# Kernel optimization log

Hardware: AMD Instinct MI355X
Metric: run time of the kernel (lower is better)

Reference implementation:

```python
import jax, jax.numpy as jnp
import numpy as np

N_NODES = 50000
N_EDGES = 300000
N_GRAPHS = 256
F_IN = 78
H1 = 10
F_H1 = 78
F_OUT = 128
NEG_SLOPE = 0.2  # PyG GATConv default leaky_relu slope


def gat_conv(x, src, dst, W, a_src, a_dst, bias, heads, out_dim):
    """PyG GATConv (eval mode): linear -> per-edge attention -> segment softmax over
    destination nodes -> scatter-add aggregation -> concat heads + bias.
    src/dst already include self-loops."""
    N = x.shape[0]
    h = (x @ W).reshape(N, heads, out_dim)              # [N,H,F]
    al_s = (h * a_src[None]).sum(-1)                     # [N,H]
    al_d = (h * a_dst[None]).sum(-1)                     # [N,H]
    e = jax.nn.leaky_relu(al_s[src] + al_d[dst], NEG_SLOPE)  # [E,H]
    m = jax.ops.segment_max(e, dst, num_segments=N)      # stable softmax per dst node
    w = jnp.exp(e - m[dst])
    denom = jax.ops.segment_sum(w, dst, num_segments=N)
    alpha = w / denom[dst]                               # [E,H]
    out = jax.ops.segment_sum(h[src] * alpha[:, :, None], dst, num_segments=N)
    return out.reshape(N, heads * out_dim) + bias


def setup_inputs() -> dict:
    key = jax.random.key(0)
    ks = jax.random.split(key, 16)
    x = jax.random.normal(ks[0], (N_NODES, F_IN), dtype=jnp.float32)
    edge_index = jax.random.randint(ks[1], (2, N_EDGES), 0, N_NODES, dtype=jnp.int32)
    batch = jnp.sort(jax.random.randint(ks[2], (N_NODES,), 0, N_GRAPHS, dtype=jnp.int32))
    s = 0.1
    W1 = jax.random.normal(ks[3], (F_IN, H1 * F_H1), dtype=jnp.float32) * s
    a_src1 = jax.random.normal(ks[4], (H1, F_H1), dtype=jnp.float32) * s
    a_dst1 = jax.random.normal(ks[5], (H1, F_H1), dtype=jnp.float32) * s
    b1 = jnp.zeros((H1 * F_H1,), dtype=jnp.float32)
    W2 = jax.random.normal(ks[6], (H1 * F_H1, F_OUT), dtype=jnp.float32) * s
    a_src2 = jax.random.normal(ks[7], (1, F_OUT), dtype=jnp.float32) * s
    a_dst2 = jax.random.normal(ks[8], (1, F_OUT), dtype=jnp.float32) * s
    b2 = jnp.zeros((F_OUT,), dtype=jnp.float32)
    fc_w = jax.random.normal(ks[9], (F_OUT, F_OUT), dtype=jnp.float32) * s
    fc_b = jnp.zeros((F_OUT,), dtype=jnp.float32)
    return dict(x=x, edge_index=edge_index, batch=batch, W1=W1, a_src1=a_src1,
                a_dst1=a_dst1, b1=b1, W2=W2, a_src2=a_src2, a_dst2=a_dst2, b2=b2,
                fc_w=fc_w, fc_b=fc_b)


def reference(x, edge_index, batch, W1, a_src1, a_dst1, b1, W2, a_src2, a_dst2, b2, fc_w, fc_b):
    N = x.shape[0]
    loop = jnp.arange(N, dtype=edge_index.dtype)
    src = jnp.concatenate([edge_index[0], loop])  # add self-loops (PyG default)
    dst = jnp.concatenate([edge_index[1], loop])
    # dropout layers are identity in eval mode
    h = jax.nn.elu(gat_conv(x, src, dst, W1, a_src1, a_dst1, b1, H1, F_H1))
    h = gat_conv(h, src, dst, W2, a_src2, a_dst2, b2, 1, F_OUT)
    h = jax.nn.relu(h)
    g = jax.ops.segment_max(h, batch, num_segments=N_GRAPHS)  # global max pool [B,F]
    out = jax.nn.relu(g @ fc_w + fc_b)
    return out
```

## Files before the change

kernel.cpp:

```cpp
#include <hip/hip_runtime.h>
#include <hip/hip_bf16.h>

#define N_NODES 50000
#define N_EDGES 300000
#define E_TOT   350000
#define N_GRAPHS 256
#define F_IN 78
#define H1 10
#define D1 780
#define F_OUT 128
#define KP 800
#define K1P 96
#define NEG_SLOPE 0.2f
#define NB 196

typedef float v4f __attribute__((ext_vector_type(4)));
typedef short v8s __attribute__((ext_vector_type(8)));

__device__ __forceinline__ int src_of(int e, const int* __restrict__ ei) {
  return (e < N_EDGES) ? ei[e] : (e - N_EDGES);
}
__device__ __forceinline__ int dst_of(int e, const int* __restrict__ ei) {
  return (e < N_EDGES) ? ei[N_EDGES + e] : (e - N_EDGES);
}


__global__ void k_deg(const int* __restrict__ ei, int* __restrict__ deg) {
  int e = blockIdx.x * 256 + threadIdx.x;
  if (e >= E_TOT) return;
  atomicAdd(&deg[dst_of(e, ei)], 1);
}

__global__ void k_scan1(const int* __restrict__ deg, int* __restrict__ part) {
  __shared__ int s[256];
  int t = threadIdx.x;
  int i = blockIdx.x * 256 + t;
  s[t] = (i < N_NODES) ? deg[i] : 0;
  __syncthreads();
  for (int d = 128; d > 0; d >>= 1) {
    if (t < d) s[t] += s[t + d];
    __syncthreads();
  }
  if (t == 0) part[blockIdx.x] = s[0];
}

__global__ void k_scan2(const int* __restrict__ part, int* __restrict__ ppref) {
  if (threadIdx.x == 0) {
    int run = 0;
    for (int i = 0; i < NB; ++i) { ppref[i] = run; run += part[i]; }
  }
}

__global__ void k_scan3(const int* __restrict__ deg, const int* __restrict__ ppref,
                        int* __restrict__ offs, int* __restrict__ cursor) {
  __shared__ int s[256];
  int t = threadIdx.x;
  int i = blockIdx.x * 256 + t;
  int v = (i < N_NODES) ? deg[i] : 0;
  s[t] = v;
  __syncthreads();
  for (int d = 1; d < 256; d <<= 1) {
    int u = (t >= d) ? s[t - d] : 0;
    __syncthreads();
    s[t] += u;
    __syncthreads();
  }
  int excl = s[t] - v;
  if (i < N_NODES) {
    int off = ppref[blockIdx.x] + excl;
    offs[i] = off;
    cursor[i] = off;
  }
}

__global__ void k_scatter(const int* __restrict__ ei, int* __restrict__ cursor,
                          int* __restrict__ src_s, int* __restrict__ dst_s) {
  int e = blockIdx.x * 256 + threadIdx.x;
  if (e >= E_TOT) return;
  int s = src_of(e, ei);
  int d = dst_of(e, ei);
  int pos = atomicAdd(&cursor[d], 1);
  src_s[pos] = s;
  dst_s[pos] = d;
}


__global__ void k_prep(const float* __restrict__ W1, const float* __restrict__ as1,
                       const float* __restrict__ ad1, float* __restrict__ was,
                       float* __restrict__ wad) {
  int i = blockIdx.x * 256 + threadIdx.x;
  if (i >= F_IN * H1) return;
  int k = i / H1, h = i - k * H1;
  const float* wrow = W1 + (size_t)k * D1 + h * 78;
  const float* ar = as1 + h * 78;
  const float* br = ad1 + h * 78;
  float s = 0.f, d = 0.f;
  for (int f = 0; f < 78; ++f) {
    float w = wrow[f];
    s = fmaf(w, ar[f], s);
    d = fmaf(w, br[f], d);
  }
  was[i] = s;
  wad[i] = d;
}


__global__ __launch_bounds__(320) void k_logits1(const float* __restrict__ x,
                                                 const float* __restrict__ was,
                                                 const float* __restrict__ wad,
                                                 float* __restrict__ als,
                                                 float* __restrict__ ald) {
  __shared__ float xs[32][81];
  __shared__ float wl[D1], wl2[D1];
  int tid = threadIdx.x;
  int n0 = blockIdx.x * 32;
  for (int i = tid; i < 32 * F_IN; i += 320) {
    int r = i / F_IN, k = i - r * F_IN;
    int n = n0 + r;
    xs[r][k] = (n < N_NODES) ? x[(size_t)n * F_IN + k] : 0.f;
  }
  for (int i = tid; i < D1; i += 320) { wl[i] = was[i]; wl2[i] = wad[i]; }
  __syncthreads();
  int r = tid / 10, h = tid - r * 10;
  int n = n0 + r;
  float s = 0.f, d = 0.f;
  for (int k = 0; k < F_IN; ++k) {
    float xv = xs[r][k];
    s = fmaf(xv, wl[k * 10 + h], s);
    d = fmaf(xv, wl2[k * 10 + h], d);
  }
  if (n < N_NODES) { als[n * 10 + h] = s; ald[n * 10 + h] = d; }
}


__global__ void k_w1e(const float* __restrict__ als1, const float* __restrict__ ald1,
                      const int* __restrict__ src_s, const int* __restrict__ dst_s,
                      float* __restrict__ w1) {
  int i = blockIdx.x * 256 + threadIdx.x;
  if (i >= E_TOT * H1) return;
  int pos = i / H1, h = i - pos * H1;
  float v = als1[src_s[pos] * H1 + h] + ald1[dst_s[pos] * H1 + h];
  v = (v > 0.f) ? v : NEG_SLOPE * v;
  w1[i] = __expf(v);
}


__global__ void k_w1t(const float* __restrict__ W1, __hip_bfloat16* __restrict__ T) {
  int i = blockIdx.x * 256 + threadIdx.x;
  if (i >= 800 * K1P) return;
  int r = i / K1P, k = i - r * K1P;
  float v = (r < D1 && k < F_IN) ? W1[(size_t)k * D1 + r] : 0.f;
  T[i] = __float2bfloat16(v);
}


__global__ void k_w2t(const float* __restrict__ W2, __hip_bfloat16* __restrict__ Bt) {
  int i = blockIdx.x * 256 + threadIdx.x;
  if (i >= F_OUT * KP) return;
  int c = i / KP, k = i - c * KP;
  float v = (k < D1) ? W2[(size_t)k * F_OUT + c] : 0.f;
  Bt[i] = __float2bfloat16(v);
}


__global__ __launch_bounds__(512, 4) void k_l12(const float* __restrict__ x,
                                                const float* __restrict__ w1,
                                                const int* __restrict__ src_s,
                                                const int* __restrict__ offs,
                                                const int* __restrict__ deg,
                                                const __hip_bfloat16* __restrict__ W1T,
                                                const float* __restrict__ b1,
                                                const __hip_bfloat16* __restrict__ W2T,
                                                const float* __restrict__ a_src2,
                                                const float* __restrict__ a_dst2,
                                                float* __restrict__ h2,
                                                float* __restrict__ als2,
                                                float* __restrict__ ald2) {
  __shared__ __align__(16) unsigned char lds[33792];
  __hip_bfloat16* xbb = (__hip_bfloat16*)lds;
  __hip_bfloat16* out1t = (__hip_bfloat16*)lds;
  float* h2t = (float*)(lds + 25600);
#define XB(h, g, k) xbb[((h) * 16 + (g)) * 104 + (k)]

  int tid = threadIdx.x, wid = tid >> 6, lane = tid & 63;
  int n0 = blockIdx.x * 16;
  int col16 = lane & 15, kq = (lane >> 4) * 8;

  {
    unsigned int* p = (unsigned int*)lds;
    for (int i = tid; i < H1 * 16 * 52; i += 512) p[i] = 0u;
  }
  __syncthreads();

  #pragma unroll
  for (int rep = 0; rep < 2; ++rep) {
    int g = wid * 2 + rep;
    int n = n0 + g;
    int o = __builtin_amdgcn_readfirstlane(offs[n]);
    int d = __builtin_amdgcn_readfirstlane(deg[n]);
    float acc[H1], acc2[H1];
    #pragma unroll
    for (int h = 0; h < H1; ++h) { acc[h] = 0.f; acc2[h] = 0.f; }

    float onesel = (lane == 14) ? 1.0f : 0.f;
    int j = 0;
    for (; j + 4 <= d; j += 4) {
      int e0 = o + j;
      int s0 = src_s[e0], s1 = src_s[e0 + 1], s2 = src_s[e0 + 2], s3 = src_s[e0 + 3];
      const float* x0 = x + (size_t)s0 * F_IN;
      const float* x1 = x + (size_t)s1 * F_IN;
      const float* x2 = x + (size_t)s2 * F_IN;
      const float* x3 = x + (size_t)s3 * F_IN;
      float xa0 = x0[lane], xa1 = x1[lane], xa2 = x2[lane], xa3 = x3[lane];
      float xb0 = (lane < 14) ? x0[64 + lane] : onesel;
      float xb1 = (lane < 14) ? x1[64 + lane] : onesel;
      float xb2 = (lane < 14) ? x2[64 + lane] : onesel;
      float xb3 = (lane < 14) ? x3[64 + lane] : onesel;
      const float* wp = w1 + (size_t)e0 * H1;
      #pragma unroll
      for (int h = 0; h < H1; ++h) {
        float wa = wp[h], wb = wp[10 + h], wc = wp[20 + h], wd = wp[30 + h];
        acc[h] = fmaf(wa, xa0, acc[h]);
        acc[h] = fmaf(wb, xa1, acc[h]);
        acc[h] = fmaf(wc, xa2, acc[h]);
        acc[h] = fmaf(wd, xa3, acc[h]);
        acc2[h] = fmaf(wa, xb0, acc2[h]);
        acc2[h] = fmaf(wb, xb1, acc2[h]);
        acc2[h] = fmaf(wc, xb2, acc2[h]);
        acc2[h] = fmaf(wd, xb3, acc2[h]);
      }
    }
    for (; j < d; ++j) {
      int e0 = o + j;
      int s0 = src_s[e0];
      const float* x0 = x + (size_t)s0 * F_IN;
      float xa0 = x0[lane];
      float xb0 = (lane < 14) ? x0[64 + lane] : onesel;
      const float* wp = w1 + (size_t)e0 * H1;
      #pragma unroll
      for (int h = 0; h < H1; ++h) {
        float wa = wp[h];
        acc[h] = fmaf(wa, xa0, acc[h]);
        acc2[h] = fmaf(wa, xb0, acc2[h]);
      }
    }
    #pragma unroll
    for (int h = 0; h < H1; ++h) {
      float inv = 1.f / __shfl(acc2[h], 14);
      XB(h, g, lane) = __float2bfloat16(acc[h] * inv);
      if (lane < 14) XB(h, g, 64 + lane) = __float2bfloat16(acc2[h] * inv);
    }
  }
  __syncthreads();

  const unsigned short* Bp1 = (const unsigned short*)W1T;
  v4f res[7];
  int nu = 0;
  for (int u = wid; u < 50; u += 8) {
    int h = u / 5, nt = u - (u / 5) * 5;
    v4f acc = (v4f){0.f, 0.f, 0.f, 0.f};
    #pragma unroll
    for (int kt = 0; kt < 3; ++kt) {
      v8s a = *reinterpret_cast<const v8s*>(&XB(h, col16, kt * 32 + kq));
      v8s b = *reinterpret_cast<const v8s*>(
          &Bp1[(size_t)(h * 78 + nt * 16 + col16) * K1P + kt * 32 + kq]);
      acc = __builtin_amdgcn_mfma_f32_16x16x32_bf16(a, b, acc, 0, 0, 0);
    }
    res[nu++] = acc;
  }
  __syncthreads();

  if (tid < 160) {
    int node = tid / 10, cc = (tid - node * 10) * 2;
    *(unsigned int*)&out1t[node * 800 + 780 + cc] = 0u;
  }
  nu = 0;
  for (int u = wid; u < 50; u += 8) {
    int h = u / 5, nt = u - (u / 5) * 5;
    v4f acc = res[nu++];
    int cl = nt * 16 + col16;
    if (cl < 78) {
      int c = h * 78 + cl;
      float bv = b1[c];
      #pragma unroll
      for (int r = 0; r < 4; ++r) {
        int node = (lane >> 4) * 4 + r;
        float v = acc[r] + bv;
        v = (v > 0.f) ? v : expm1f(v);
        out1t[node * 800 + c] = __float2bfloat16(v);
      }
    }
  }
  __syncthreads();

  const unsigned short* Bp2 = (const unsigned short*)W2T;
  v4f acc3 = (v4f){0.f, 0.f, 0.f, 0.f};
  #pragma unroll 5
  for (int kt = 0; kt < 25; ++kt) {
    int k = kt * 32 + kq;
    v8s a = *reinterpret_cast<const v8s*>(&out1t[col16 * 800 + k]);
    v8s b = *reinterpret_cast<const v8s*>(&Bp2[(size_t)(wid * 16 + col16) * KP + k]);
    acc3 = __builtin_amdgcn_mfma_f32_16x16x32_bf16(a, b, acc3, 0, 0, 0);
  }
  {
    int col = wid * 16 + col16;
    #pragma unroll
    for (int r = 0; r < 4; ++r) {
      int node = (lane >> 4) * 4 + r;
      h2[(size_t)(n0 + node) * F_OUT + col] = acc3[r];
      h2t[node * F_OUT + col] = acc3[r];
    }
  }
  __syncthreads();

  #pragma unroll
  for (int rep = 0; rep < 2; ++rep) {
    int nn = wid * 2 + rep;
    float v0 = h2t[nn * F_OUT + lane], v1 = h2t[nn * F_OUT + 64 + lane];
    float s = v0 * a_src2[lane] + v1 * a_src2[64 + lane];
    float dd = v0 * a_dst2[lane] + v1 * a_dst2[64 + lane];
    #pragma unroll
    for (int off = 32; off > 0; off >>= 1) {
      s += __shfl_down(s, off);
      dd += __shfl_down(dd, off);
    }
    if (lane == 0) { als2[n0 + nn] = s; ald2[n0 + nn] = dd; }
  }
#undef XB
}


__global__ void k_w2e(const float* __restrict__ als2, const float* __restrict__ ald2,
                      const int* __restrict__ src_s, const int* __restrict__ dst_s,
                      float* __restrict__ w2) {
  int pos = blockIdx.x * 256 + threadIdx.x;
  if (pos >= E_TOT) return;
  float v = als2[src_s[pos]] + ald2[dst_s[pos]];
  v = (v > 0.f) ? v : NEG_SLOPE * v;
  w2[pos] = __expf(v);
}


__global__ __launch_bounds__(512) void k_agg2f(const float* __restrict__ h2,
                                               const float* __restrict__ w2,
                                               const int* __restrict__ src_s,
                                               const int* __restrict__ offs,
                                               const int* __restrict__ deg,
                                               const float* __restrict__ b2,
                                               const int* __restrict__ batch,
                                               unsigned int* __restrict__ g) {
  int tid = threadIdx.x;
  int n = blockIdx.x * 4 + (tid >> 7);
  int f = tid & 127;
  int o = __builtin_amdgcn_readfirstlane(offs[n]);
  int d = __builtin_amdgcn_readfirstlane(deg[n]);
  float acc = 0.f, ssum = 0.f;
  int j = 0;
  for (; j + 4 <= d; j += 4) {
    float wq[4], hq[4];
    #pragma unroll
    for (int q = 0; q < 4; ++q) {
      int e = o + j + q;
      wq[q] = w2[e];
      hq[q] = h2[(size_t)src_s[e] * F_OUT + f];
    }
    #pragma unroll
    for (int q = 0; q < 4; ++q) {
      ssum += wq[q];
      acc = fmaf(wq[q], hq[q], acc);
    }
  }
  for (; j < d; ++j) {
    int e = o + j;
    float w = w2[e];
    ssum += w;
    acc = fmaf(w, h2[(size_t)src_s[e] * F_OUT + f], acc);
  }
  float v = fmaxf(acc / ssum + b2[f], 0.f);
  int gc = __builtin_amdgcn_readfirstlane(batch[n]);
  atomicMax(&g[gc * F_OUT + f], __float_as_uint(v));
}


__global__ __launch_bounds__(128) void k_fc(const float* __restrict__ g,
                                            const float* __restrict__ fc_w,
                                            const float* __restrict__ fc_b,
                                            float* __restrict__ out) {
  int b = blockIdx.x, c = threadIdx.x;
  const float* gr = g + (size_t)b * F_OUT;
  float acc = 0.f;
  for (int k = 0; k < F_OUT; ++k) acc = fmaf(gr[k], fc_w[k * F_OUT + c], acc);
  float v = acc + fc_b[c];
  out[(size_t)b * F_OUT + c] = fmaxf(v, 0.f);
}


extern "C" void kernel_launch(void* const* d_in, const int* in_sizes, int n_in,
                              void* d_out, int out_size, void* d_ws, size_t ws_size,
                              hipStream_t stream) {
  const float* x      = (const float*)d_in[0];
  const int*   ei     = (const int*)  d_in[1];
  const int*   batch  = (const int*)  d_in[2];
  const float* W1     = (const float*)d_in[3];
  const float* a_src1 = (const float*)d_in[4];
  const float* a_dst1 = (const float*)d_in[5];
  const float* b1     = (const float*)d_in[6];
  const float* W2     = (const float*)d_in[7];
  const float* a_src2 = (const float*)d_in[8];
  const float* a_dst2 = (const float*)d_in[9];
  const float* b2     = (const float*)d_in[10];
  const float* fc_w   = (const float*)d_in[11];
  const float* fc_b   = (const float*)d_in[12];
  float* out = (float*)d_out;

  float* ws = (float*)d_ws;
  float* h2   = ws;
  float* als1 = ws + 6400000;
  float* ald1 = ws + 6900000;
  float* als2 = ws + 7400000;
  float* ald2 = ws + 7450000;
  float* g    = ws + 7500000;
  float* was  = ws + 7533000;
  float* wad  = ws + 7534000;
  __hip_bfloat16* W2T = (__hip_bfloat16*)(ws + 7535000);
  __hip_bfloat16* W1T = (__hip_bfloat16*)(ws + 7587000);
  float* w1   = ws + 7626000;
  float* w2   = ws + 11126000;
  int* ib     = (int*)(ws + 11476000);
  int* deg    = ib;
  int* offs   = ib + 50000;
  int* cursor = ib + 100000;
  int* src_s  = ib + 150000;
  int* dst_s  = ib + 500000;
  int* part   = ib + 850000;
  int* ppref  = ib + 850224;

  hipMemsetAsync(deg, 0, N_NODES * sizeof(int), stream);
  k_deg<<<(E_TOT + 255) / 256, 256, 0, stream>>>(ei, deg);
  k_scan1<<<NB, 256, 0, stream>>>(deg, part);
  k_scan2<<<1, 64, 0, stream>>>(part, ppref);
  k_scan3<<<NB, 256, 0, stream>>>(deg, ppref, offs, cursor);
  k_scatter<<<(E_TOT + 255) / 256, 256, 0, stream>>>(ei, cursor, src_s, dst_s);

  k_prep<<<4, 256, 0, stream>>>(W1, a_src1, a_dst1, was, wad);
  k_w1t<<<(800 * K1P + 255) / 256, 256, 0, stream>>>(W1, W1T);
  k_w2t<<<(F_OUT * KP + 255) / 256, 256, 0, stream>>>(W2, W2T);
  hipMemsetAsync(g, 0, N_GRAPHS * F_OUT * sizeof(float), stream);

  k_logits1<<<(N_NODES + 31) / 32, 320, 0, stream>>>(x, was, wad, als1, ald1);
  k_w1e<<<(E_TOT * H1 + 255) / 256, 256, 0, stream>>>(als1, ald1, src_s, dst_s, w1);

  k_l12<<<N_NODES / 16, 512, 0, stream>>>(x, w1, src_s, offs, deg, W1T, b1,
                                          W2T, a_src2, a_dst2, h2, als2, ald2);

  k_w2e<<<(E_TOT + 255) / 256, 256, 0, stream>>>(als2, ald2, src_s, dst_s, w2);
  k_agg2f<<<(N_NODES + 3) / 4, 512, 0, stream>>>(h2, w2, src_s, offs, deg, b2, batch, (unsigned int*)g);

  k_fc<<<N_GRAPHS, F_OUT, 0, stream>>>(g, fc_w, fc_b, out);
}
```

Measured before the change: 269.7 us.

## Store gathered node features and layer-2 projections in bf16 to halve gather traffic

Adds a pre-pass that converts x to bf16, so the layer-1 edge aggregation gathers bf16 rows. The layer-2 projection h2 is also written in bf16 and read as bf16 in the final aggregation. The aim is to roughly halve the bytes moved by the random per-edge gathers, at the cost of an extra conversion kernel and reduced precision. It also pads the LDS row stride (808) to cut bank conflicts in the second MFMA and fully unrolls the first MFMA loop so res[] stays in registers.

```diff
diff --git a/kernel.cpp b/kernel.cpp
--- a/kernel.cpp
+++ b/kernel.cpp
@@ -11,6 +11,7 @@
 #define F_OUT 128
 #define KP 800
 #define K1P 96
+#define O1P 808
 #define NEG_SLOPE 0.2f
 #define NB 196
 
@@ -22,6 +23,9 @@
 }
 __device__ __forceinline__ int dst_of(int e, const int* __restrict__ ei) {
   return (e < N_EDGES) ? ei[N_EDGES + e] : (e - N_EDGES);
+}
+__device__ __forceinline__ float bf2f(unsigned short u) {
+  return __uint_as_float(((unsigned int)u) << 16);
 }
 
 
@@ -82,6 +86,13 @@
   int pos = atomicAdd(&cursor[d], 1);
   src_s[pos] = s;
   dst_s[pos] = d;
+}
+
+
+__global__ void k_xb(const float* __restrict__ x, __hip_bfloat16* __restrict__ xb) {
+  int i = blockIdx.x * 256 + threadIdx.x;
+  if (i >= N_NODES * F_IN) return;
+  xb[i] = __float2bfloat16(x[i]);
 }
 
 
@@ -163,7 +174,7 @@
 }
 
 
-__global__ __launch_bounds__(512, 4) void k_l12(const float* __restrict__ x,
+__global__ __launch_bounds__(512, 4) void k_l12(const __hip_bfloat16* __restrict__ xb16,
                                                 const float* __restrict__ w1,
                                                 const int* __restrict__ src_s,
                                                 const int* __restrict__ offs,
@@ -173,13 +184,13 @@
                                                 const __hip_bfloat16* __restrict__ W2T,
                                                 const float* __restrict__ a_src2,
                                                 const float* __restrict__ a_dst2,
-                                                float* __restrict__ h2,
+                                                __hip_bfloat16* __restrict__ h2b,
                                                 float* __restrict__ als2,
                                                 float* __restrict__ ald2) {
-  __shared__ __align__(16) unsigned char lds[33792];
+  __shared__ __align__(16) unsigned char lds[34048];
   __hip_bfloat16* xbb = (__hip_bfloat16*)lds;
   __hip_bfloat16* out1t = (__hip_bfloat16*)lds;
-  float* h2t = (float*)(lds + 25600);
+  float* h2t = (float*)(lds + 25856);
 #define XB(h, g, k) xbb[((h) * 16 + (g)) * 104 + (k)]
 
   int tid = threadIdx.x, wid = tid >> 6, lane = tid & 63;
@@ -203,19 +214,21 @@
     for (int h = 0; h < H1; ++h) { acc[h] = 0.f; acc2[h] = 0.f; }
 
     float onesel = (lane == 14) ? 1.0f : 0.f;
+    const unsigned short* xu = (const unsigned short*)xb16;
     int j = 0;
     for (; j + 4 <= d; j += 4) {
       int e0 = o + j;
       int s0 = src_s[e0], s1 = src_s[e0 + 1], s2 = src_s[e0 + 2], s3 = src_s[e0 + 3];
-      const float* x0 = x + (size_t)s0 * F_IN;
-      const float* x1 = x + (size_t)s1 * F_IN;
-      const float* x2 = x + (size_t)s2 * F_IN;
-      const float* x3 = x + (size_t)s3 * F_IN;
-      float xa0 = x0[lane], xa1 = x1[lane], xa2 = x2[lane], xa3 = x3[lane];
-      float xb0 = (lane < 14) ? x0[64 + lane] : onesel;
-      float xb1 = (lane < 14) ? x1[64 + lane] : onesel;
-      float xb2 = (lane < 14) ? x2[64 + lane] : onesel;
-      float xb3 = (lane < 14) ? x3[64 + lane] : onesel;
+      const unsigned short* x0 = xu + (size_t)s0 * F_IN;
+      const unsigned short* x1 = xu + (size_t)s1 * F_IN;
+      const unsigned short* x2 = xu + (size_t)s2 * F_IN;
+      const unsigned short* x3 = xu + (size_t)s3 * F_IN;
+      float xa0 = bf2f(x0[lane]), xa1 = bf2f(x1[lane]);
+      float xa2 = bf2f(x2[lane]), xa3 = bf2f(x3[lane]);
+      float xb0 = (lane < 14) ? bf2f(x0[64 + lane]) : onesel;
+      float xb1 = (lane < 14) ? bf2f(x1[64 + lane]) : onesel;
+      float xb2 = (lane < 14) ? bf2f(x2[64 + lane]) : onesel;
+      float xb3 = (lane < 14) ? bf2f(x3[64 + lane]) : onesel;
       const float* wp = w1 + (size_t)e0 * H1;
       #pragma unroll
       for (int h = 0; h < H1; ++h) {
@@ -233,9 +246,9 @@
     for (; j < d; ++j) {
       int e0 = o + j;
       int s0 = src_s[e0];
-      const float* x0 = x + (size_t)s0 * F_IN;
-      float xa0 = x0[lane];
-      float xb0 = (lane < 14) ? x0[64 + lane] : onesel;
+      const unsigned short* x0 = xu + (size_t)s0 * F_IN;
+      float xa0 = bf2f(x0[lane]);
+      float xb0 = (lane < 14) ? bf2f(x0[64 + lane]) : onesel;
       const float* wp = w1 + (size_t)e0 * H1;
       #pragma unroll
       for (int h = 0; h < H1; ++h) {
@@ -255,39 +268,45 @@
 
   const unsigned short* Bp1 = (const unsigned short*)W1T;
   v4f res[7];
-  int nu = 0;
-  for (int u = wid; u < 50; u += 8) {
-    int h = u / 5, nt = u - (u / 5) * 5;
+  #pragma unroll
+  for (int i = 0; i < 7; ++i) {
+    int u = wid + i * 8;
     v4f acc = (v4f){0.f, 0.f, 0.f, 0.f};
-    #pragma unroll
-    for (int kt = 0; kt < 3; ++kt) {
-      v8s a = *reinterpret_cast<const v8s*>(&XB(h, col16, kt * 32 + kq));
-      v8s b = *reinterpret_cast<const v8s*>(
-          &Bp1[(size_t)(h * 78 + nt * 16 + col16) * K1P + kt * 32 + kq]);
-      acc = __builtin_amdgcn_mfma_f32_16x16x32_bf16(a, b, acc, 0, 0, 0);
-    }
-    res[nu++] = acc;
-  }
-  __syncthreads();
-
-  if (tid < 160) {
-    int node = tid / 10, cc = (tid - node * 10) * 2;
-    *(unsigned int*)&out1t[node * 800 + 780 + cc] = 0u;
-  }
-  nu = 0;
-  for (int u = wid; u < 50; u += 8) {
-    int h = u / 5, nt = u - (u / 5) * 5;
-    v4f acc = res[nu++];
-    int cl = nt * 16 + col16;
-    if (cl < 78) {
-      int c = h * 78 + cl;
-      float bv = b1[c];
+    if (u < 50) {
+      int h = u / 5, nt = u - (u / 5) * 5;
       #pragma unroll
-      for (int r = 0; r < 4; ++r) {
-        int node = (lane >> 4) * 4 + r;
-        float v = acc[r] + bv;
-        v = (v > 0.f) ? v : expm1f(v);
-        out1t[node * 800 + c] = __float2bfloat16(v);
+      for (int kt = 0; kt < 3; ++kt) {
+        v8s a = *reinterpret_cast<const v8s*>(&XB(h, col16, kt * 32 + kq));
+        v8s b = *reinterpret_cast<const v8s*>(
+            &Bp1[(size_t)(h * 78 + nt * 16 + col16) * K1P + kt * 32 + kq]);
+        acc = __builtin_amdgcn_mfma_f32_16x16x32_bf16(a, b, acc, 0, 0, 0);
+      }
+    }
+    res[i] = acc;
+  }
+  __syncthreads();
+
+  if (tid < 224) {
+    int node = tid / 14, cc = (tid - node * 14) * 2;
+    *(unsigned int*)&out1t[node * O1P + 780 + cc] = 0u;
+  }
+  #pragma unroll
+  for (int i = 0; i < 7; ++i) {
+    int u = wid + i * 8;
+    if (u < 50) {
+      int h = u / 5, nt = u - (u / 5) * 5;
+      v4f acc = res[i];
+      int cl = nt * 16 + col16;
+      if (cl < 78) {
+        int c = h * 78 + cl;
+        float bv = b1[c];
+        #pragma unroll
+        for (int r = 0; r < 4; ++r) {
+          int node = (lane >> 4) * 4 + r;
+          float v = acc[r] + bv;
+          v = (v > 0.f) ? v : expm1f(v);
+          out1t[node * O1P + c] = __float2bfloat16(v);
+        }
       }
     }
   }
@@ -298,7 +317,7 @@
   #pragma unroll 5
   for (int kt = 0; kt < 25; ++kt) {
     int k = kt * 32 + kq;
-    v8s a = *reinterpret_cast<const v8s*>(&out1t[col16 * 800 + k]);
+    v8s a = *reinterpret_cast<const v8s*>(&out1t[col16 * O1P + k]);
     v8s b = *reinterpret_cast<const v8s*>(&Bp2[(size_t)(wid * 16 + col16) * KP + k]);
     acc3 = __builtin_amdgcn_mfma_f32_16x16x32_bf16(a, b, acc3, 0, 0, 0);
   }
@@ -307,7 +326,7 @@
     #pragma unroll
     for (int r = 0; r < 4; ++r) {
       int node = (lane >> 4) * 4 + r;
-      h2[(size_t)(n0 + node) * F_OUT + col] = acc3[r];
+      h2b[(size_t)(n0 + node) * F_OUT + col] = __float2bfloat16(acc3[r]);
       h2t[node * F_OUT + col] = acc3[r];
     }
   }
@@ -341,7 +360,7 @@
 }
 
 
-__global__ __launch_bounds__(512) void k_agg2f(const float* __restrict__ h2,
+__global__ __launch_bounds__(512) void k_agg2f(const __hip_bfloat16* __restrict__ h2b,
                                                const float* __restrict__ w2,
                                                const int* __restrict__ src_s,
                                                const int* __restrict__ offs,
@@ -354,6 +373,7 @@
   int f = tid & 127;
   int o = __builtin_amdgcn_readfirstlane(offs[n]);
   int d = __builtin_amdgcn_readfirstlane(deg[n]);
+  const unsigned short* hu = (const unsigned short*)h2b;
   float acc = 0.f, ssum = 0.f;
   int j = 0;
   for (; j + 4 <= d; j += 4) {
@@ -362,7 +382,7 @@
     for (int q = 0; q < 4; ++q) {
       int e = o + j + q;
       wq[q] = w2[e];
-      hq[q] = h2[(size_t)src_s[e] * F_OUT + f];
+      hq[q] = bf2f(hu[(size_t)src_s[e] * F_OUT + f]);
     }
     #pragma unroll
     for (int q = 0; q < 4; ++q) {
@@ -374,7 +394,7 @@
     int e = o + j;
     float w = w2[e];
     ssum += w;
-    acc = fmaf(w, h2[(size_t)src_s[e] * F_OUT + f], acc);
+    acc = fmaf(w, bf2f(hu[(size_t)src_s[e] * F_OUT + f]), acc);
   }
   float v = fmaxf(acc / ssum + b2[f], 0.f);
   int gc = __builtin_amdgcn_readfirstlane(batch[n]);
@@ -414,19 +434,20 @@
   float* out = (float*)d_out;
 
   float* ws = (float*)d_ws;
-  float* h2   = ws;
-  float* als1 = ws + 6400000;
-  float* ald1 = ws + 6900000;
-  float* als2 = ws + 7400000;
-  float* ald2 = ws + 7450000;
-  float* g    = ws + 7500000;
-  float* was  = ws + 7533000;
-  float* wad  = ws + 7534000;
-  __hip_bfloat16* W2T = (__hip_bfloat16*)(ws + 7535000);
-  __hip_bfloat16* W1T = (__hip_bfloat16*)(ws + 7587000);
-  float* w1   = ws + 7626000;
-  float* w2   = ws + 11126000;
-  int* ib     = (int*)(ws + 11476000);
+  __hip_bfloat16* h2b = (__hip_bfloat16*)ws;
+  float* als1 = ws + 3200000;
+  float* ald1 = ws + 3700000;
+  float* als2 = ws + 4200000;
+  float* ald2 = ws + 4250000;
+  float* g    = ws + 4300000;
+  float* was  = ws + 4333000;
+  float* wad  = ws + 4334000;
+  __hip_bfloat16* W2T = (__hip_bfloat16*)(ws + 4335000);
+  __hip_bfloat16* W1T = (__hip_bfloat16*)(ws + 4387000);
+  __hip_bfloat16* xb16 = (__hip_bfloat16*)(ws + 4426000);
+  float* w1   = ws + 6377000;
+  float* w2   = ws + 9877000;
+  int* ib     = (int*)(ws + 10227000);
   int* deg    = ib;
   int* offs   = ib + 50000;
   int* cursor = ib + 100000;
@@ -445,16 +466,17 @@
   k_prep<<<4, 256, 0, stream>>>(W1, a_src1, a_dst1, was, wad);
   k_w1t<<<(800 * K1P + 255) / 256, 256, 0, stream>>>(W1, W1T);
   k_w2t<<<(F_OUT * KP + 255) / 256, 256, 0, stream>>>(W2, W2T);
+  k_xb<<<(N_NODES * F_IN + 255) / 256, 256, 0, stream>>>(x, xb16);
   hipMemsetAsync(g, 0, N_GRAPHS * F_OUT * sizeof(float), stream);
 
   k_logits1<<<(N_NODES + 31) / 32, 320, 0, stream>>>(x, was, wad, als1, ald1);
   k_w1e<<<(E_TOT * H1 + 255) / 256, 256, 0, stream>>>(als1, ald1, src_s, dst_s, w1);
 
-  k_l12<<<N_NODES / 16, 512, 0, stream>>>(x, w1, src_s, offs, deg, W1T, b1,
-                                          W2T, a_src2, a_dst2, h2, als2, ald2);
+  k_l12<<<N_NODES / 16, 512, 0, stream>>>(xb16, w1, src_s, offs, deg, W1T, b1,
+                                          W2T, a_src2, a_dst2, h2b, als2, ald2);
 
   k_w2e<<<(E_TOT + 255) / 256, 256, 0, stream>>>(als2, ald2, src_s, dst_s, w2);
-  k_agg2f<<<(N_NODES + 3) / 4, 512, 0, stream>>>(h2, w2, src_s, offs, deg, b2, batch, (unsigned int*)g);
+  k_agg2f<<<(N_NODES + 3) / 4, 512, 0, stream>>>(h2b, w2, src_s, offs, deg, b2, batch, (unsigned int*)g);
 
   k_fc<<<N_GRAPHS, F_OUT, 0, stream>>>(g, fc_w, fc_b, out);
 }
```

New measurement: 311.6 us. 1.16x slower.
